# Kernel optimization log

Hardware: AMD Instinct MI355X
Metric: run time of the kernel (lower is better)

Reference implementation:

```python
import jax, jax.numpy as jnp
import numpy as np

GAMMA = 20.0
NUM_VIEWS = 64

def setup_inputs() -> dict:
    key = jax.random.key(0)
    k1, k2, k3 = jax.random.split(key, 3)
    B, L, D = 16, 4096, 1024
    v_pad = jax.random.normal(k1, (B, L, D), dtype=jnp.float32)
    v_len = jax.random.randint(k2, (B,), 1, L + 1, dtype=jnp.int32)
    # (T, H, W) per sample; only W/H ratio matters -> square 64x64 grid
    grid_thws = jnp.tile(jnp.array([[1, 64, 64]], dtype=jnp.int32), (B, 1))
    centers = jax.random.uniform(k3, (B, NUM_VIEWS, 2), dtype=jnp.float32)
    return {"v_pad": v_pad, "v_len": v_len, "grid_thws": grid_thws, "centers": centers}

def reference(v_pad, v_len, grid_thws, centers):
    B, L, D = v_pad.shape
    Lv = v_len.astype(jnp.float32)                      # [B]
    H = grid_thws[:, 1].astype(jnp.float32)
    W = grid_thws[:, 2].astype(jnp.float32)
    # adaptive 2D mapping of the 1D token sequence
    W_eff = jnp.maximum(1, jnp.round(jnp.sqrt(Lv * (W / H))).astype(jnp.int32))  # [B]
    H_eff = jnp.maximum(1, jnp.ceil(Lv / W_eff.astype(jnp.float32)).astype(jnp.int32))
    idx = jnp.arange(L, dtype=jnp.int32)                # [L]
    We = W_eff[:, None]
    He = H_eff[:, None]
    x = (idx[None, :] % We).astype(jnp.float32) / We.astype(jnp.float32)   # [B, L]
    y = (idx[None, :] // We).astype(jnp.float32) / He.astype(jnp.float32)  # [B, L]
    coords = jnp.stack([x, y], axis=-1)                 # [B, L, 2]
    # squared distance from each view center to each token coord
    diff = centers[:, :, None, :] - coords[:, None, :, :]   # [B, V, L, 2]
    dist_sq = jnp.sum(diff * diff, axis=-1)                 # [B, V, L]
    valid = (idx[None, :] < v_len[:, None]).astype(v_pad.dtype)  # [B, L]
    m = jnp.exp(-GAMMA * dist_sq) * valid[:, None, :]       # [B, V, L]
    numerator = jnp.einsum('bvl,bld->bvd', m, v_pad)        # [B, V, D]
    denominator = jnp.sum(m, axis=-1, keepdims=True) + 1e-6 # [B, V, 1]
    return numerator / denominator
```

## Files before the change

kernel.cpp:

```cpp
#include <hip/hip_runtime.h>
#include <hip/hip_bf16.h>
#include <math.h>
#include <stdint.h>


constexpr int VV  = 64;
constexpr int DC  = 128;
constexpr int KS  = 64;
constexpr int NTH = 256;
constexpr int ST2 = 134;
constexpr int KCH = 8;

typedef __attribute__((ext_vector_type(8))) short short8;
typedef __attribute__((ext_vector_type(4))) float f32x4;
typedef _Float16 f16;
typedef __attribute__((ext_vector_type(4))) _Float16 f16x4;

static __device__ __forceinline__ unsigned short f2bf(float f) {
    __hip_bfloat16 h = __float2bfloat16(f);
    return __builtin_bit_cast(unsigned short, h);
}

__global__ __launch_bounds__(256)
void dvs_prep(const int* __restrict__ v_len, const int* __restrict__ gthw,
              const float* __restrict__ centers,
              unsigned short* __restrict__ mws,
              float* __restrict__ den_tile,
              int NT)
{
    const int t = blockIdx.x, b = blockIdx.y;
    const int Lv = v_len[b];
    const int lt = t * KS;
    if (lt >= Lv) return;

    const float Hf = (float)gthw[b*3 + 1];
    const float Wf = (float)gthw[b*3 + 2];
    const float sq = sqrtf((float)Lv * (Wf / Hf));
    int W_eff = (int)rintf(sq);                       if (W_eff < 1) W_eff = 1;
    int H_eff = (int)ceilf((float)Lv / (float)W_eff); if (H_eff < 1) H_eff = 1;
    const float invW = 1.f / (float)W_eff, invH = 1.f / (float)H_eff;

    const int tid  = threadIdx.x;
    const int lane = tid & 63, wave = tid >> 6;
    const int ar = lane & 15, koct = lane >> 4;

    __shared__ float sden[2][4][VV];

    short8* mtile = (short8*)mws + ((size_t)b * NT + t) * 8 * 64;

#pragma unroll
    for (int i = 0; i < 2; ++i) {
        const int f  = wave * 2 + i;
        const int ks = f >> 2, mf = f & 3;
        const int v  = mf * 16 + ar;
        const float2 ctr = ((const float2*)centers)[(size_t)b * VV + v];

        int l   = lt + ks * 32 + koct * 8;
        int row = l / W_eff;
        int col = l - row * W_eff;
        float y = (float)row * invH;

        union { unsigned short h[8]; short8 s; } ap;
        float ds = 0.f;
#pragma unroll
        for (int j = 0; j < 8; ++j) {
            float m = 0.f;
            if (l + j < Lv) {
                const float x  = (float)col * invW;
                const float dx = ctr.x - x, dy = ctr.y - y;
                m = __expf(-20.f * (dx * dx + dy * dy));
            }
            ds += m;
            ap.h[j] = f2bf(m);
            if (++col == W_eff) { col = 0; ++row; y = (float)row * invH; }
        }
        mtile[f * 64 + lane] = ap.s;
        sden[ks][koct][v] = ds;
    }
    __syncthreads();
    if (tid < VV) {
        float s = 0.f;
#pragma unroll
        for (int ks = 0; ks < 2; ++ks)
#pragma unroll
            for (int q = 0; q < 4; ++q) s += sden[ks][q][tid];
        den_tile[((size_t)b * NT + t) * VV + tid] = s;
    }
}

__global__ __launch_bounds__(NTH)
void dvs_mfma(const float* __restrict__ v_pad, const int* __restrict__ v_len,
              const unsigned short* __restrict__ mws,
              f16* __restrict__ num_part,
              int L, int D, int NT)
{
    const int flat = blockIdx.x;
    const int kblk = flat >> 7;
    const int g    = flat & 127;
    const int dcb  = g & 7;
    const int b    = g >> 3;

    const int Lv = v_len[b];
    const int chunk = (((Lv + KCH - 1) / KCH) + 63) & ~63;
    const int l0 = kblk * chunk;
    if (l0 >= Lv) return;
    const int l1 = min(l0 + chunk, Lv);

    const int tid  = threadIdx.x;
    const int d0   = dcb * DC;
    const int lane = tid & 63;
    const int wave = tid >> 6;

    __shared__ __align__(16) unsigned short smB[KS][ST2];

    const int sd   = tid & 31;
    const int srow = tid >> 5;
    const int fcol = lane & 15, foct = lane >> 4;

    f32x4 acc[4][2];
#pragma unroll
    for (int i = 0; i < 4; ++i) {
        acc[i][0] = f32x4{0.f, 0.f, 0.f, 0.f};
        acc[i][1] = f32x4{0.f, 0.f, 0.f, 0.f};
    }

    const float*  vp_b  = v_pad + (size_t)b * L * D + d0;
    const short8* mws_b = (const short8*)mws + (size_t)b * NT * 8 * 64;

    float4 ld[8];
#pragma unroll
    for (int it = 0; it < 8; ++it) {
        const int l = l0 + it * 8 + srow;
        ld[it] = make_float4(0.f, 0.f, 0.f, 0.f);
        if (l < l1)
            ld[it] = *(const float4*)(vp_b + (size_t)l * D + sd * 4);
    }

    for (int lt = l0; lt < l1; lt += KS) {
#pragma unroll
        for (int it = 0; it < 8; ++it) {
            const int lrow = it * 8 + srow;
            unsigned* w = (unsigned*)&smB[lrow][sd * 4];
            w[0] = (unsigned)f2bf(ld[it].x) | ((unsigned)f2bf(ld[it].y) << 16);
            w[1] = (unsigned)f2bf(ld[it].z) | ((unsigned)f2bf(ld[it].w) << 16);
        }
        __syncthreads();

        const int ltn = lt + KS;
        if (ltn < l1) {
#pragma unroll
            for (int it = 0; it < 8; ++it) {
                const int l = ltn + it * 8 + srow;
                ld[it] = make_float4(0.f, 0.f, 0.f, 0.f);
                if (l < l1)
                    ld[it] = *(const float4*)(vp_b + (size_t)l * D + sd * 4);
            }
        }

        const short8* mt = mws_b + ((size_t)(lt >> 6)) * 8 * 64;
        short8 af[2][4];
#pragma unroll
        for (int ks = 0; ks < 2; ++ks)
#pragma unroll
            for (int mf = 0; mf < 4; ++mf)
                af[ks][mf] = mt[(ks * 4 + mf) * 64 + lane];

#pragma unroll
        for (int ks = 0; ks < 2; ++ks) {
#pragma unroll
            for (int nf = 0; nf < 2; ++nf) {
                const int colx  = wave * 32 + nf * 16 + fcol;
                const int kbase = ks * 32 + foct * 8;
                union { unsigned short h[8]; short8 s; } bf;
#pragma unroll
                for (int j = 0; j < 8; ++j)
                    bf.h[j] = smB[kbase + j][colx];
#pragma unroll
                for (int mf = 0; mf < 4; ++mf)
                    acc[mf][nf] = __builtin_amdgcn_mfma_f32_16x16x32_bf16(
                        af[ks][mf], bf.s, acc[mf][nf], 0, 0, 0);
            }
        }
        __syncthreads();
    }

    f16* basep = num_part + ((size_t)b * KCH + kblk) * VV * (size_t)D + d0 + wave * 32;
#pragma unroll
    for (int mf = 0; mf < 4; ++mf) {
#pragma unroll
        for (int nf = 0; nf < 2; ++nf) {
            const int colx = nf * 16 + fcol;
            const int row0 = mf * 16 + foct * 4;
#pragma unroll
            for (int r = 0; r < 4; ++r)
                basep[(size_t)(row0 + r) * D + colx] = (f16)acc[mf][nf][r];
        }
    }
}

__global__ __launch_bounds__(256)
void dvs_reduce(const f16* __restrict__ num_part,
                const float* __restrict__ den_tile,
                const int*   __restrict__ v_len,
                float*       __restrict__ out,
                int D, int NT)
{
    const int flat = blockIdx.x;
    const int vg  = flat >> 7;
    const int gg  = flat & 127;
    const int dcb = gg & 7;
    const int b   = gg >> 3;

    const int tid = threadIdx.x;
    const int vi  = tid >> 5;
    const int c4  = tid & 31;
    const int v   = vg * 8 + vi;

    const int Lv    = v_len[b];
    const int chunk = (((Lv + KCH - 1) / KCH) + 63) & ~63;
    const int nk    = (Lv + chunk - 1) / chunk;
    const int nt    = (Lv + KS - 1) / KS;

    __shared__ float sp[8][8];
    __shared__ float sinv[8];
    if (tid < 64) {
        const int vd = vg * 8 + (tid & 7);
        const int part = tid >> 3;
        float s = 0.f;
        for (int t = part; t < nt; t += 8)
            s += den_tile[((size_t)b * NT + t) * VV + vd];
        sp[tid & 7][part] = s;
    }
    __syncthreads();
    if (tid < 8) {
        float s = 1e-6f;
#pragma unroll
        for (int p = 0; p < 8; ++p) s += sp[tid][p];
        sinv[tid] = 1.0f / s;
    }
    __syncthreads();

    const int dof = dcb * DC + c4 * 4;
    float4 num = make_float4(0.f, 0.f, 0.f, 0.f);
    for (int k = 0; k < nk; ++k) {
        const f16x4 p = *(const f16x4*)(num_part +
            (((size_t)b * KCH + k) * VV + v) * (size_t)D + dof);
        num.x += (float)p[0]; num.y += (float)p[1];
        num.z += (float)p[2]; num.w += (float)p[3];
    }
    const float inv = sinv[vi];
    *(float4*)(out + ((size_t)b * VV + v) * (size_t)D + dof) =
        make_float4(num.x * inv, num.y * inv, num.z * inv, num.w * inv);
}

extern "C" void kernel_launch(void* const* d_in, const int* in_sizes, int n_in,
                              void* d_out, int out_size, void* d_ws, size_t ws_size,
                              hipStream_t stream)
{
    const float* v_pad     = (const float*)d_in[0];
    const int*   v_len     = (const int*)d_in[1];
    const int*   grid_thws = (const int*)d_in[2];
    const float* centers   = (const float*)d_in[3];
    float*       out       = (float*)d_out;

    const int B  = in_sizes[1];
    const int D  = out_size / (B * VV);
    const int L  = in_sizes[0] / (B * D);
    const int NT = (L + KS - 1) / KS;

    f16*            num_part = (f16*)d_ws;
    float*          den_tile = (float*)(num_part + (size_t)B * KCH * VV * D);
    unsigned short* mws      = (unsigned short*)(den_tile + (size_t)B * NT * VV);

    dim3 gridP(NT, B);
    dvs_prep<<<gridP, 256, 0, stream>>>(v_len, grid_thws, centers, mws,
                                        den_tile, NT);

    const int nblkG = KCH * (D / DC) * B;
    dvs_mfma<<<nblkG, NTH, 0, stream>>>(v_pad, v_len, mws, num_part, L, D, NT);

    const int nblkR = 8 * (D / DC) * B;
    dvs_reduce<<<nblkR, 256, 0, stream>>>(num_part, den_tile, v_len, out, D, NT);
}
```

Measured before the change: 48.27 us.

## Fuse split-K reduction into MFMA kernel via last-block atomic counter

Removes the separate reduce kernel. Each MFMA block now writes fp32 partials, bumps a per-(batch, D-chunk) atomic counter, and the last block to finish sums the partials, computes the denominators and writes the normalized output. The prep kernel resets the counters. This saves one kernel launch and the extra pass over the partials, but the last block does a serial reduction and the partials now take twice the bytes in fp32 instead of fp16.

```diff
diff --git a/kernel.cpp b/kernel.cpp
--- a/kernel.cpp
+++ b/kernel.cpp
@@ -13,8 +13,6 @@
 
 typedef __attribute__((ext_vector_type(8))) short short8;
 typedef __attribute__((ext_vector_type(4))) float f32x4;
-typedef _Float16 f16;
-typedef __attribute__((ext_vector_type(4))) _Float16 f16x4;
 
 static __device__ __forceinline__ unsigned short f2bf(float f) {
     __hip_bfloat16 h = __float2bfloat16(f);
@@ -26,9 +24,13 @@
               const float* __restrict__ centers,
               unsigned short* __restrict__ mws,
               float* __restrict__ den_tile,
+              int* __restrict__ flags,
               int NT)
 {
     const int t = blockIdx.x, b = blockIdx.y;
+    if (t == 0 && threadIdx.x < 8)
+        flags[b * 8 + threadIdx.x] = 0;
+
     const int Lv = v_len[b];
     const int lt = t * KS;
     if (lt >= Lv) return;
@@ -91,7 +93,10 @@
 __global__ __launch_bounds__(NTH)
 void dvs_mfma(const float* __restrict__ v_pad, const int* __restrict__ v_len,
               const unsigned short* __restrict__ mws,
-              f16* __restrict__ num_part,
+              const float* __restrict__ den_tile,
+              float* __restrict__ num_part,
+              int* __restrict__ flags,
+              float* __restrict__ out,
               int L, int D, int NT)
 {
     const int flat = blockIdx.x;
@@ -102,6 +107,7 @@
 
     const int Lv = v_len[b];
     const int chunk = (((Lv + KCH - 1) / KCH) + 63) & ~63;
+    const int nk = (Lv + chunk - 1) / chunk;
     const int l0 = kblk * chunk;
     if (l0 >= Lv) return;
     const int l1 = min(l0 + chunk, Lv);
@@ -112,6 +118,8 @@
     const int wave = tid >> 6;
 
     __shared__ __align__(16) unsigned short smB[KS][ST2];
+    __shared__ int   s_last;
+    __shared__ float sinv[VV];
 
     const int sd   = tid & 31;
     const int srow = tid >> 5;
@@ -184,7 +192,7 @@
         __syncthreads();
     }
 
-    f16* basep = num_part + ((size_t)b * KCH + kblk) * VV * (size_t)D + d0 + wave * 32;
+    float* basep = num_part + ((size_t)b * KCH + kblk) * VV * (size_t)D + d0 + wave * 32;
 #pragma unroll
     for (int mf = 0; mf < 4; ++mf) {
 #pragma unroll
@@ -193,64 +201,42 @@
             const int row0 = mf * 16 + foct * 4;
 #pragma unroll
             for (int r = 0; r < 4; ++r)
-                basep[(size_t)(row0 + r) * D + colx] = (f16)acc[mf][nf][r];
-        }
-    }
-}
-
-__global__ __launch_bounds__(256)
-void dvs_reduce(const f16* __restrict__ num_part,
-                const float* __restrict__ den_tile,
-                const int*   __restrict__ v_len,
-                float*       __restrict__ out,
-                int D, int NT)
-{
-    const int flat = blockIdx.x;
-    const int vg  = flat >> 7;
-    const int gg  = flat & 127;
-    const int dcb = gg & 7;
-    const int b   = gg >> 3;
-
-    const int tid = threadIdx.x;
-    const int vi  = tid >> 5;
-    const int c4  = tid & 31;
-    const int v   = vg * 8 + vi;
-
-    const int Lv    = v_len[b];
-    const int chunk = (((Lv + KCH - 1) / KCH) + 63) & ~63;
-    const int nk    = (Lv + chunk - 1) / chunk;
-    const int nt    = (Lv + KS - 1) / KS;
-
-    __shared__ float sp[8][8];
-    __shared__ float sinv[8];
-    if (tid < 64) {
-        const int vd = vg * 8 + (tid & 7);
-        const int part = tid >> 3;
+                basep[(size_t)(row0 + r) * D + colx] = acc[mf][nf][r];
+        }
+    }
+
+    __threadfence();
+    __syncthreads();
+    if (tid == 0)
+        s_last = (atomicAdd(&flags[g], 1) == nk - 1);
+    __syncthreads();
+    if (!s_last) return;
+    __threadfence();
+
+    const int nt = (Lv + KS - 1) / KS;
+    if (tid < VV) {
         float s = 0.f;
-        for (int t = part; t < nt; t += 8)
-            s += den_tile[((size_t)b * NT + t) * VV + vd];
-        sp[tid & 7][part] = s;
-    }
-    __syncthreads();
-    if (tid < 8) {
-        float s = 1e-6f;
-#pragma unroll
-        for (int p = 0; p < 8; ++p) s += sp[tid][p];
-        sinv[tid] = 1.0f / s;
-    }
-    __syncthreads();
-
-    const int dof = dcb * DC + c4 * 4;
-    float4 num = make_float4(0.f, 0.f, 0.f, 0.f);
-    for (int k = 0; k < nk; ++k) {
-        const f16x4 p = *(const f16x4*)(num_part +
-            (((size_t)b * KCH + k) * VV + v) * (size_t)D + dof);
-        num.x += (float)p[0]; num.y += (float)p[1];
-        num.z += (float)p[2]; num.w += (float)p[3];
-    }
-    const float inv = sinv[vi];
-    *(float4*)(out + ((size_t)b * VV + v) * (size_t)D + dof) =
-        make_float4(num.x * inv, num.y * inv, num.z * inv, num.w * inv);
+        const float* dt = den_tile + (size_t)b * NT * VV + tid;
+        for (int t = 0; t < nt; ++t) s += dt[(size_t)t * VV];
+        sinv[tid] = 1.0f / (s + 1e-6f);
+    }
+    __syncthreads();
+
+    const int c4 = tid & 31;
+    const int vb = tid >> 5;
+    const float* np_b = num_part + (size_t)b * KCH * VV * D + d0 + c4 * 4;
+#pragma unroll
+    for (int i = 0; i < 8; ++i) {
+        const int v = vb * 8 + i;
+        float4 s = make_float4(0.f, 0.f, 0.f, 0.f);
+        for (int k = 0; k < nk; ++k) {
+            const float4 p = *(const float4*)(np_b + ((size_t)k * VV + v) * D);
+            s.x += p.x; s.y += p.y; s.z += p.z; s.w += p.w;
+        }
+        const float inv = sinv[v];
+        *(float4*)(out + ((size_t)b * VV + v) * D + d0 + c4 * 4) =
+            make_float4(s.x * inv, s.y * inv, s.z * inv, s.w * inv);
+    }
 }
 
 extern "C" void kernel_launch(void* const* d_in, const int* in_sizes, int n_in,
@@ -268,17 +254,16 @@
     const int L  = in_sizes[0] / (B * D);
     const int NT = (L + KS - 1) / KS;
 
-    f16*            num_part = (f16*)d_ws;
-    float*          den_tile = (float*)(num_part + (size_t)B * KCH * VV * D);
+    float*          num_part = (float*)d_ws;
+    float*          den_tile = num_part + (size_t)B * KCH * VV * D;
     unsigned short* mws      = (unsigned short*)(den_tile + (size_t)B * NT * VV);
+    int*            flags    = (int*)(mws + (size_t)B * NT * 8 * 64 * 8);
 
     dim3 gridP(NT, B);
     dvs_prep<<<gridP, 256, 0, stream>>>(v_len, grid_thws, centers, mws,
-                                        den_tile, NT);
+                                        den_tile, flags, NT);
 
     const int nblkG = KCH * (D / DC) * B;
-    dvs_mfma<<<nblkG, NTH, 0, stream>>>(v_pad, v_len, mws, num_part, L, D, NT);
-
-    const int nblkR = 8 * (D / DC) * B;
-    dvs_reduce<<<nblkR, 256, 0, stream>>>(num_part, den_tile, v_len, out, D, NT);
-}
+    dvs_mfma<<<nblkG, NTH, 0, stream>>>(v_pad, v_len, mws, den_tile,
+                                        num_part, flags, out, L, D, NT);
+}
```

Measured after the change: 191.8 us. 297% more time.
